# Kernel tuning notes

Hardware: AMD Instinct MI355X
Metric: run time of the kernel (lower is better)

## Reference

```python
import jax, jax.numpy as jnp
import numpy as np
from jax import lax

EPS = 1e-8

def _cosine_cost(x, y):
    # 1 - cosine_similarity over feature dim: [B,N,M]
    xn = x / jnp.clip(jnp.linalg.norm(x, axis=-1, keepdims=True), EPS)
    yn = y / jnp.clip(jnp.linalg.norm(y, axis=-1, keepdims=True), EPS)
    return 1.0 - jnp.einsum('bnd,bmd->bnm', xn, yn)

def _dtw_table(cost):
    # cost: [B,N,M] -> cumulative cost tc: [B,N,M]
    # tc[i,j] = cost[i,j] + min(tc[i-1,j-1], tc[i-1,j], tc[i,j-1])
    B, N, M = cost.shape
    row0 = jnp.cumsum(cost[:, 0, :], axis=1)  # [B,M]

    def col_step(left, inp):
        c, pdiag, pup = inp  # each [B]
        v = c + jnp.minimum(jnp.minimum(pdiag, pup), left)
        return v, v

    def row_step(prev, cost_row):
        # prev, cost_row: [B,M]
        first = prev[:, 0] + cost_row[:, 0]  # [B]
        xs = (cost_row[:, 1:].T, prev[:, :-1].T, prev[:, 1:].T)  # [M-1,B]
        _, rest = lax.scan(col_step, first, xs)  # [M-1,B]
        row = jnp.concatenate([first[:, None], rest.T], axis=1)  # [B,M]
        return row, row

    _, rows = lax.scan(row_step, row0, jnp.swapaxes(cost[:, 1:, :], 0, 1))
    tc = jnp.concatenate([row0[:, None, :], jnp.swapaxes(rows, 0, 1)], axis=1)
    return tc

def _backtrack(tc):
    # tc: [N,M] -> 0/1 path matrix [N,M]; tie-break diag > up > left,
    # matching the torch equality-chain order.
    N, M = tc.shape
    path0 = jnp.zeros((N, M), tc.dtype).at[N - 1, M - 1].set(1.0)

    def cond(s):
        i, j, _ = s
        return jnp.logical_and(i > 0, j > 0)

    def body(s):
        i, j, p = s
        a = tc[i - 1, j - 1]
        b = tc[i - 1, j]
        c = tc[i, j - 1]
        diag = jnp.logical_and(a <= b, a <= c)
        up = jnp.logical_and(jnp.logical_not(diag), b <= c)
        ni = jnp.where(jnp.logical_or(diag, up), i - 1, i)
        nj = jnp.where(jnp.logical_or(diag, jnp.logical_not(up)), j - 1, j)
        p = p.at[ni, nj].set(1.0)
        return ni, nj, p

    _, _, p = lax.while_loop(cond, body, (jnp.int32(N - 1), jnp.int32(M - 1), path0))
    return p.at[0, 0].set(1.0)

def setup_inputs() -> dict:
    key = jax.random.key(0)
    kx, ky = jax.random.split(key)
    B, N, M, D = 64, 512, 512, 256
    x = jax.random.normal(kx, (B, N, D), dtype=jnp.float32)
    y = jax.random.normal(ky, (B, M, D), dtype=jnp.float32)
    return {"x": x, "y": y}

def reference(x, y):
    cost = _cosine_cost(x, y)                 # [B,N,M]
    tc = _dtw_table(cost)                     # [B,N,M]
    path = jax.vmap(_backtrack)(tc)           # [B,N,M]
    pos = jax.nn.logsumexp(jnp.sum(cost * path, axis=1), axis=1)  # [B]
    neg = jax.nn.logsumexp(jnp.sum(cost, axis=1), axis=1)         # [B]
    return pos - neg
```

## Files before the change

### kernel.cpp

```cpp
#include <hip/hip_runtime.h>
#include <hip/hip_bf16.h>
#include <stdint.h>

typedef __attribute__((ext_vector_type(8))) short short8v;
typedef __attribute__((ext_vector_type(4))) float float4v;
typedef __attribute__((ext_vector_type(4))) unsigned short ushort4v;
typedef __attribute__((ext_vector_type(4))) unsigned int uint4v;

#define FINF __builtin_huge_valf()
#define BB 64
#define NN 512
#define DD 256
#define TT_SKEW 768


static __device__ __forceinline__ unsigned short f2bf(float f) {
  union { float f; uint32_t u; } a; a.f = f;
  uint32_t r = a.u + 0x7fffu + ((a.u >> 16) & 1u);
  return (unsigned short)(r >> 16);
}
static __device__ __forceinline__ float bf2f(uint16_t v) {
  return __uint_as_float(((uint32_t)v) << 16);
}

__global__ __launch_bounds__(256) void zero_colsum_kernel(float* __restrict__ colsum)
{
  colsum[blockIdx.x * 256 + threadIdx.x] = 0.0f;
}

__global__ __launch_bounds__(256) void norm_cast_kernel(
    const float* __restrict__ x, const float* __restrict__ y,
    uint16_t* __restrict__ xnb, uint16_t* __restrict__ ynb)
{
  const int wave = threadIdx.x >> 6, lane = threadIdx.x & 63;
  const int row = blockIdx.x * 4 + wave;
  const float* src; uint16_t* dst;
  if (row < BB * NN) { src = x + (size_t)row * DD;            dst = xnb + (size_t)row * DD; }
  else               { src = y + (size_t)(row - BB*NN) * DD;  dst = ynb + (size_t)(row - BB*NN) * DD; }
  const float4v v = *(const float4v*)(src + lane * 4);
  float s = v[0]*v[0] + v[1]*v[1] + v[2]*v[2] + v[3]*v[3];
  #pragma unroll
  for (int d = 1; d < 64; d <<= 1) s += __shfl_xor(s, d, 64);
  const float inv = 1.0f / fmaxf(sqrtf(s), 1e-8f);
  ushort4v o;
  o[0] = f2bf(v[0] * inv); o[1] = f2bf(v[1] * inv);
  o[2] = f2bf(v[2] * inv); o[3] = f2bf(v[3] * inv);
  *(ushort4v*)(dst + lane * 4) = o;
}

__global__ __launch_bounds__(256) void gemm_cost_kernel(
    const uint16_t* __restrict__ xnb, const uint16_t* __restrict__ ynb,
    uint16_t* __restrict__ skew, float* __restrict__ colsum)
{
  __shared__ uint16_t As[128 * 32];
  __shared__ uint16_t Bs[128 * 32];
  const int bid = blockIdx.x;
  const int b = bid >> 4, tm = (bid >> 2) & 3, tn = bid & 3;
  const int tid = threadIdx.x, wave = tid >> 6, lane = tid & 63;
  const int wr = wave >> 1, wc = wave & 1;

  const char* Ab = (const char*)(xnb + (size_t)b * NN * DD + (size_t)tm * 128 * DD);
  const char* Bb = (const char*)(ynb + (size_t)b * NN * DD + (size_t)tn * 128 * DD);

  float4v acc[4][4];
  #pragma unroll
  for (int i = 0; i < 4; i++)
    #pragma unroll
    for (int j = 0; j < 4; j++) acc[i][j] = (float4v){0.f, 0.f, 0.f, 0.f};

  const int seg0 = wave * 2;
  const int o0 = seg0 * 1024 + lane * 16;
  const int o1 = o0 + 1024;
  const int r0 = o0 >> 6, c0 = o0 & 63;
  const int r1 = o1 >> 6, c1 = o1 & 63;

  for (int kk = 0; kk < 8; kk++) {
    const int kb = kk * 64;
    __builtin_amdgcn_global_load_lds(
        (const __attribute__((address_space(1))) uint32_t*)(Ab + (size_t)r0 * 512 + kb + c0),
        (__attribute__((address_space(3))) uint32_t*)((char*)As + seg0 * 1024), 16, 0, 0);
    __builtin_amdgcn_global_load_lds(
        (const __attribute__((address_space(1))) uint32_t*)(Ab + (size_t)r1 * 512 + kb + c1),
        (__attribute__((address_space(3))) uint32_t*)((char*)As + (seg0 + 1) * 1024), 16, 0, 0);
    __builtin_amdgcn_global_load_lds(
        (const __attribute__((address_space(1))) uint32_t*)(Bb + (size_t)r0 * 512 + kb + c0),
        (__attribute__((address_space(3))) uint32_t*)((char*)Bs + seg0 * 1024), 16, 0, 0);
    __builtin_amdgcn_global_load_lds(
        (const __attribute__((address_space(1))) uint32_t*)(Bb + (size_t)r1 * 512 + kb + c1),
        (__attribute__((address_space(3))) uint32_t*)((char*)Bs + (seg0 + 1) * 1024), 16, 0, 0);
    __syncthreads();

    short8v af[4], bfr[4];
    #pragma unroll
    for (int mi = 0; mi < 4; mi++) {
      const int rr = wr * 64 + mi * 16 + (lane & 15);
      af[mi] = *(const short8v*)((const char*)As + rr * 64 + (lane >> 4) * 16);
    }
    #pragma unroll
    for (int nj = 0; nj < 4; nj++) {
      const int rr = wc * 64 + nj * 16 + (lane & 15);
      bfr[nj] = *(const short8v*)((const char*)Bs + rr * 64 + (lane >> 4) * 16);
    }
    #pragma unroll
    for (int mi = 0; mi < 4; mi++)
      #pragma unroll
      for (int nj = 0; nj < 4; nj++)
        acc[mi][nj] = __builtin_amdgcn_mfma_f32_16x16x32_bf16(af[mi], bfr[nj], acc[mi][nj], 0, 0, 0);
    __syncthreads();
  }

  uint16_t* Cb = skew + (size_t)b * TT_SKEW * NN;
  #pragma unroll
  for (int mi = 0; mi < 4; mi++)
    #pragma unroll
    for (int nj = 0; nj < 4; nj++) {
      const int cc = tn * 128 + wc * 64 + nj * 16 + (lane & 15);
      const int lg = cc >> 3;
      #pragma unroll
      for (int v = 0; v < 4; v++) {
        const int rr = tm * 128 + wr * 64 + mi * 16 + (lane >> 4) * 4 + v;
        Cb[(size_t)(rr + 4 * lg) * NN + cc] = f2bf(1.0f - acc[mi][nj][v]);
      }
    }

  #pragma unroll
  for (int nj = 0; nj < 4; nj++) {
    const int cc = tn * 128 + wc * 64 + nj * 16 + (lane & 15);
    float s = 0.f;
    #pragma unroll
    for (int mi = 0; mi < 4; mi++)
      #pragma unroll
      for (int v = 0; v < 4; v++) s += 1.0f - acc[mi][nj][v];
    s += __shfl_xor(s, 16, 64);
    s += __shfl_xor(s, 32, 64);
    if (lane < 16) atomicAdd(&colsum[b * 512 + cc], s);
  }
}

__global__ __launch_bounds__(64, 1) void dtw_fwd_kernel(
    const uint16_t* __restrict__ skew, uint32_t* __restrict__ decg,
    uint32_t* __restrict__ dumpg)
{
  const int l = threadIdx.x;
  const int b = blockIdx.x;
  const uint16_t* csk = skew + (size_t)b * TT_SKEW * NN;
  uint32_t* const dw = decg + (size_t)b * 16384;
  const uint64_t base64 = (uint64_t)(uintptr_t)csk + 16u * (uint32_t)l;
  const bool is0 = (l == 0);

  uint4v rg[4][4];
  #pragma unroll
  for (int i = 0; i < 4; ++i)
    #pragma unroll
    for (int k = 0; k < 4; ++k) {
      const uint64_t a = base64 + ((uint64_t)(4 * i + k) << 10);
      asm volatile("global_load_dwordx4 %0, %1, off" : "=v"(rg[i][k]) : "v"(a));
    }

  float tp[8];
  #pragma unroll
  for (int c = 0; c < 8; ++c) tp[c] = FINF;
  float cl0 = FINF, cl1 = FINF, cl2 = FINF, cl3 = FINF, carry = FINF;

  auto UNPACK = [&](const uint4v R, float (&S)[8]) {
    const float a0 = __uint_as_float(R[0] << 16);
    const float a1 = __uint_as_float(R[0] & 0xFFFF0000u);
    const float a2 = __uint_as_float(R[1] << 16);
    const float a3 = __uint_as_float(R[1] & 0xFFFF0000u);
    const float a4 = __uint_as_float(R[2] << 16);
    const float a5 = __uint_as_float(R[2] & 0xFFFF0000u);
    const float a6 = __uint_as_float(R[3] << 16);
    const float a7 = __uint_as_float(R[3] & 0xFFFF0000u);
    S[0] = a0; S[1] = S[0] + a1; S[2] = S[1] + a2; S[3] = S[2] + a3;
    S[4] = S[3] + a4; S[5] = S[4] + a5; S[6] = S[5] + a6; S[7] = S[6] + a7;
  };

  auto ROW = [&](const float (&S)[8], float (&up)[8], float leftv, float diag0,
                 uint32_t &word, int sh) {
    float dcp[8], mu[8], w[8], PW[8], tn[8];
    dcp[0] = diag0;
    #pragma unroll
    for (int c = 1; c < 8; ++c) dcp[c] = up[c - 1];
    #pragma unroll
    for (int c = 0; c < 8; ++c) mu[c] = fminf(dcp[c], up[c]);
    w[0] = mu[0];
    #pragma unroll
    for (int c = 1; c < 8; ++c) w[c] = mu[c] - S[c - 1];
    PW[0] = w[0];
    #pragma unroll
    for (int c = 1; c < 8; ++c) PW[c] = fminf(PW[c - 1], w[c]);
    #pragma unroll
    for (int c = 0; c < 8; ++c) tn[c] = fminf(PW[c], leftv) + S[c];
    float lc[8];
    lc[0] = leftv;
    #pragma unroll
    for (int c = 1; c < 8; ++c) lc[c] = tn[c - 1];
    #pragma unroll
    for (int c = 0; c < 8; ++c) {
      const uint32_t e = (up[c] < dcp[c]) ? 1u : 0u;
      const uint32_t d = (lc[c] < mu[c]) ? 2u : e;
      word |= d << (sh + 2 * c);
    }
    #pragma unroll
    for (int c = 0; c < 8; ++c) up[c] = tn[c];
  };

  auto STEP = [&](int t, const uint4v R0, const uint4v R1,
                  const uint4v R2, const uint4v R3) {
    const float s0r = __shfl_up(cl0, 1, 64);
    const float s1r = __shfl_up(cl1, 1, 64);
    const float s2r = __shfl_up(cl2, 1, 64);
    const float s3r = __shfl_up(cl3, 1, 64);
    float S0[8], S1[8], S2[8], S3[8];
    UNPACK(R0, S0); UNPACK(R1, S1); UNPACK(R2, S2); UNPACK(R3, S3);
    const float sh0 = is0 ? ((t == 0) ? 0.0f : FINF) : s0r;
    const float sh1 = is0 ? FINF : s1r;
    const float sh2 = is0 ? FINF : s2r;
    const float sh3 = is0 ? FINF : s3r;
    const float dgA = carry;
    const float dg1 = is0 ? FINF : s0r;
    const float dg2 = is0 ? FINF : s1r;
    const float dg3 = is0 ? FINF : s2r;
    carry = sh3;

    const uint32_t a = (uint32_t)(t - l);
    const bool valid = a < 128u;

    float up[8];
    #pragma unroll
    for (int c = 0; c < 8; ++c) up[c] = tp[c];
    uint32_t w0 = 0, w1 = 0;
    ROW(S0, up, sh0, dgA, w0, 0);  const float h0 = up[7];
    ROW(S1, up, sh1, dg1, w0, 16); const float h1 = up[7];
    ROW(S2, up, sh2, dg2, w1, 0);  const float h2 = up[7];
    ROW(S3, up, sh3, dg3, w1, 16); const float h3 = up[7];

    uint32_t* p0 = valid ? (dw + (a << 7) + l) : (dumpg + l);
    uint32_t* p1 = valid ? (dw + (a << 7) + 64 + l) : (dumpg + 64 + l);
    *p0 = w0; *p1 = w1;

    #pragma unroll
    for (int c = 0; c < 8; ++c) tp[c] = valid ? up[c] : tp[c];
    cl0 = valid ? h0 : cl0;
    cl1 = valid ? h1 : cl1;
    cl2 = valid ? h2 : cl2;
    cl3 = valid ? h3 : cl3;
  };

  auto RELOAD = [&](int u, int t) {
    int rr = 4 * (t + 4); if (rr > 764) rr = 764;
    #pragma unroll
    for (int k = 0; k < 4; ++k) {
      const uint64_t a = base64 + ((uint64_t)(rr + k) << 10);
      asm volatile("global_load_dwordx4 %0, %1, off" : "=v"(rg[u][k]) : "v"(a));
    }
  };

  asm volatile("s_waitcnt vmcnt(12)"
               : "+v"(rg[0][0]), "+v"(rg[0][1]), "+v"(rg[0][2]), "+v"(rg[0][3]) : : "memory");
  STEP(0, rg[0][0], rg[0][1], rg[0][2], rg[0][3]); RELOAD(0, 0);
  asm volatile("s_waitcnt vmcnt(14)"
               : "+v"(rg[1][0]), "+v"(rg[1][1]), "+v"(rg[1][2]), "+v"(rg[1][3]) : : "memory");
  STEP(1, rg[1][0], rg[1][1], rg[1][2], rg[1][3]); RELOAD(1, 1);
  asm volatile("s_waitcnt vmcnt(16)"
               : "+v"(rg[2][0]), "+v"(rg[2][1]), "+v"(rg[2][2]), "+v"(rg[2][3]) : : "memory");
  STEP(2, rg[2][0], rg[2][1], rg[2][2], rg[2][3]); RELOAD(2, 2);
  asm volatile("s_waitcnt vmcnt(18)"
               : "+v"(rg[3][0]), "+v"(rg[3][1]), "+v"(rg[3][2]), "+v"(rg[3][3]) : : "memory");
  STEP(3, rg[3][0], rg[3][1], rg[3][2], rg[3][3]); RELOAD(3, 3);

  for (int t0 = 4; t0 < 192; t0 += 4) {
    #pragma unroll
    for (int u = 0; u < 4; ++u) {
      const int t = t0 + u;
      asm volatile("s_waitcnt vmcnt(18)"
                   : "+v"(rg[u][0]), "+v"(rg[u][1]), "+v"(rg[u][2]), "+v"(rg[u][3]) : : "memory");
      STEP(t, rg[u][0], rg[u][1], rg[u][2], rg[u][3]);
      RELOAD(u, t);
    }
  }
  asm volatile("s_waitcnt vmcnt(0)" ::: "memory");
}

__global__ __launch_bounds__(256, 1) void dtw_bt_kernel(
    const uint16_t* __restrict__ skew, const uint32_t* __restrict__ decg,
    const float* __restrict__ colsum, float* __restrict__ out)
{
  extern __shared__ char lds_raw[];
  uint16_t* rlo    = (uint16_t*)(lds_raw + 65536);
  uint16_t* rhi    = (uint16_t*)(lds_raw + 66560);
  float*    colpos = (float*)  (lds_raw + 67584);
  float*    sm     = (float*)  (lds_raw + 69632);
  const uint32_t* dec32 = (const uint32_t*)lds_raw;

  const int tid = threadIdx.x, wave = tid >> 6, lane = tid & 63;
  const int b = blockIdx.x;
  const uint16_t* csk = skew + (size_t)b * TT_SKEW * NN;
  const uint32_t* dg = decg + (size_t)b * 16384;

  #pragma unroll
  for (int i = 0; i < 16; ++i)
    *(uint4v*)(lds_raw + i * 4096 + tid * 16) = *(const uint4v*)(dg + i * 1024 + tid * 4);
  for (int r = tid; r < NN; r += 256) { rlo[r] = 1; rhi[r] = 0; colpos[r] = 0.0f; }

  const float* cs = colsum + (size_t)b * 512;
  const float n0 = cs[tid], n1 = cs[tid + 256];
  float m = fmaxf(n0, n1);
  #pragma unroll
  for (int d = 1; d < 64; d <<= 1) m = fmaxf(m, __shfl_xor(m, d, 64));
  if (lane == 0) sm[wave] = m;
  __syncthreads();
  m = fmaxf(fmaxf(sm[0], sm[1]), fmaxf(sm[2], sm[3]));
  float e = expf(n0 - m) + expf(n1 - m);
  #pragma unroll
  for (int d = 1; d < 64; d <<= 1) e += __shfl_xor(e, d, 64);
  if (lane == 0) sm[4 + wave] = e;
  __syncthreads();
  const float neg = m + logf(sm[4] + sm[5] + sm[6] + sm[7]);
  __syncthreads();

  if (tid == 0) {
    int i = NN - 1, j = NN - 1, hicur = NN - 1;
    while (i > 0 && j > 0) {
      const int a = i >> 2, g2 = j >> 3;
      const uint32_t w0 = dec32[a * 128 + g2];
      const uint32_t w1 = dec32[a * 128 + 64 + g2];
      const int ilo = a << 2, jlo = g2 << 3;
      while (i >= ilo && j >= jlo && i > 0 && j > 0) {
        const uint32_t w = (i & 2) ? w1 : w0;
        const uint32_t dd = (w >> (((i & 1) << 4) + ((j & 7) << 1))) & 3u;
        if (dd == 2u) { j--; }
        else {
          rlo[i] = (uint16_t)j; rhi[i] = (uint16_t)hicur;
          i--;
          if (dd == 0u) j--;
          hicur = j;
        }
      }
    }
    rlo[i] = (uint16_t)j; rhi[i] = (uint16_t)hicur;
  }
  __syncthreads();

  for (int r = tid; r < NN; r += 256) {
    const int lo = rlo[r], hi = rhi[r];
    for (int j = lo; j <= hi; j++) {
      const float cv = bf2f(csk[(size_t)(r + 4 * (j >> 3)) * NN + j]);
      atomicAdd(&colpos[j], cv);
    }
  }
  if (tid == 0 && rlo[0] != 0) atomicAdd(&colpos[0], bf2f(csk[0]));
  __syncthreads();

  const float mv0 = colpos[tid], mv1 = colpos[tid + 256];
  float mx = fmaxf(mv0, mv1);
  #pragma unroll
  for (int d = 1; d < 64; d <<= 1) mx = fmaxf(mx, __shfl_xor(mx, d, 64));
  if (lane == 0) sm[wave] = mx;
  __syncthreads();
  mx = fmaxf(fmaxf(sm[0], sm[1]), fmaxf(sm[2], sm[3]));
  float e2 = expf(mv0 - mx) + expf(mv1 - mx);
  #pragma unroll
  for (int d = 1; d < 64; d <<= 1) e2 += __shfl_xor(e2, d, 64);
  if (lane == 0) sm[4 + wave] = e2;
  __syncthreads();
  if (tid == 0) out[b] = mx + logf(sm[4] + sm[5] + sm[6] + sm[7]) - neg;
}

extern "C" void kernel_launch(void* const* d_in, const int* in_sizes, int n_in,
                              void* d_out, int out_size, void* d_ws, size_t ws_size,
                              hipStream_t stream)
{
  (void)in_sizes; (void)n_in; (void)out_size; (void)ws_size;
  const float* x = (const float*)d_in[0];
  const float* y = (const float*)d_in[1];
  float* out = (float*)d_out;
  char* ws = (char*)d_ws;
  uint16_t* xnb   = (uint16_t*)ws;
  uint16_t* ynb   = (uint16_t*)(ws + (size_t)16777216);
  uint16_t* skew  = (uint16_t*)(ws + (size_t)33554432);
  float*   colsum = (float*)   (ws + (size_t)83886080);
  uint32_t* dumpg = (uint32_t*)(ws + (size_t)84017152);
  uint32_t* decg  = (uint32_t*)(ws + (size_t)84021248);

  (void)hipFuncSetAttribute((const void*)dtw_bt_kernel,
                            hipFuncAttributeMaxDynamicSharedMemorySize, 69760);

  zero_colsum_kernel<<<128, 256, 0, stream>>>(colsum);
  norm_cast_kernel<<<16384, 256, 0, stream>>>(x, y, xnb, ynb);
  gemm_cost_kernel<<<1024, 256, 0, stream>>>(xnb, ynb, skew, colsum);
  dtw_fwd_kernel<<<64, 64, 0, stream>>>(skew, decg, dumpg);
  dtw_bt_kernel<<<64, 256, 69760, stream>>>(skew, decg, colsum, out);
}
```

Before: 285.6 us.

## Fuse DTW forward and backtrack kernels, keeping direction bits in LDS

Merges the DTW forward-pass kernel and the backtrack/logsumexp kernel into one 64-thread kernel per batch. The direction bits now go straight to shared memory instead of a global buffer, which removes a kernel launch and the global write and re-read of the 64KB decision table per batch. The reductions are reworked for a single wave using shuffles only. The tradeoffs are that the final path-cost gather runs with 64 threads instead of 256, and the load-wait schedule is simplified to a uniform vmcnt(12) with the memory clobber dropped.

```diff
diff --git a/kernel.cpp b/kernel.cpp
--- a/kernel.cpp
+++ b/kernel.cpp
@@ -137,14 +137,14 @@
   }
 }
 
-__global__ __launch_bounds__(64, 1) void dtw_fwd_kernel(
-    const uint16_t* __restrict__ skew, uint32_t* __restrict__ decg,
-    uint32_t* __restrict__ dumpg)
-{
+__global__ __launch_bounds__(64, 1) void dtw_fwdbt_kernel(
+    const uint16_t* __restrict__ skew, const float* __restrict__ colsum,
+    float* __restrict__ out)
+{
+  extern __shared__ char lds_raw[];
   const int l = threadIdx.x;
   const int b = blockIdx.x;
   const uint16_t* csk = skew + (size_t)b * TT_SKEW * NN;
-  uint32_t* const dw = decg + (size_t)b * 16384;
   const uint64_t base64 = (uint64_t)(uintptr_t)csk + 16u * (uint32_t)l;
   const bool is0 = (l == 0);
 
@@ -235,9 +235,10 @@
     ROW(S2, up, sh2, dg2, w1, 0);  const float h2 = up[7];
     ROW(S3, up, sh3, dg3, w1, 16); const float h3 = up[7];
 
-    uint32_t* p0 = valid ? (dw + (a << 7) + l) : (dumpg + l);
-    uint32_t* p1 = valid ? (dw + (a << 7) + 64 + l) : (dumpg + 64 + l);
-    *p0 = w0; *p1 = w1;
+    const uint32_t byte0 = valid ? ((a << 9) | (((uint32_t)l) << 2))
+                                 : (65536u | (((uint32_t)l) << 2));
+    *(uint32_t*)(lds_raw + byte0) = w0;
+    *(uint32_t*)(lds_raw + byte0 + 256) = w1;
 
     #pragma unroll
     for (int c = 0; c < 8; ++c) tp[c] = valid ? up[c] : tp[c];
@@ -256,70 +257,41 @@
     }
   };
 
-  asm volatile("s_waitcnt vmcnt(12)"
-               : "+v"(rg[0][0]), "+v"(rg[0][1]), "+v"(rg[0][2]), "+v"(rg[0][3]) : : "memory");
-  STEP(0, rg[0][0], rg[0][1], rg[0][2], rg[0][3]); RELOAD(0, 0);
-  asm volatile("s_waitcnt vmcnt(14)"
-               : "+v"(rg[1][0]), "+v"(rg[1][1]), "+v"(rg[1][2]), "+v"(rg[1][3]) : : "memory");
-  STEP(1, rg[1][0], rg[1][1], rg[1][2], rg[1][3]); RELOAD(1, 1);
-  asm volatile("s_waitcnt vmcnt(16)"
-               : "+v"(rg[2][0]), "+v"(rg[2][1]), "+v"(rg[2][2]), "+v"(rg[2][3]) : : "memory");
-  STEP(2, rg[2][0], rg[2][1], rg[2][2], rg[2][3]); RELOAD(2, 2);
-  asm volatile("s_waitcnt vmcnt(18)"
-               : "+v"(rg[3][0]), "+v"(rg[3][1]), "+v"(rg[3][2]), "+v"(rg[3][3]) : : "memory");
-  STEP(3, rg[3][0], rg[3][1], rg[3][2], rg[3][3]); RELOAD(3, 3);
-
-  for (int t0 = 4; t0 < 192; t0 += 4) {
+  for (int t0 = 0; t0 < 192; t0 += 4) {
     #pragma unroll
     for (int u = 0; u < 4; ++u) {
       const int t = t0 + u;
-      asm volatile("s_waitcnt vmcnt(18)"
-                   : "+v"(rg[u][0]), "+v"(rg[u][1]), "+v"(rg[u][2]), "+v"(rg[u][3]) : : "memory");
+      asm volatile("s_waitcnt vmcnt(12)"
+                   : "+v"(rg[u][0]), "+v"(rg[u][1]), "+v"(rg[u][2]), "+v"(rg[u][3]));
       STEP(t, rg[u][0], rg[u][1], rg[u][2], rg[u][3]);
       RELOAD(u, t);
     }
   }
   asm volatile("s_waitcnt vmcnt(0)" ::: "memory");
-}
-
-__global__ __launch_bounds__(256, 1) void dtw_bt_kernel(
-    const uint16_t* __restrict__ skew, const uint32_t* __restrict__ decg,
-    const float* __restrict__ colsum, float* __restrict__ out)
-{
-  extern __shared__ char lds_raw[];
-  uint16_t* rlo    = (uint16_t*)(lds_raw + 65536);
-  uint16_t* rhi    = (uint16_t*)(lds_raw + 66560);
-  float*    colpos = (float*)  (lds_raw + 67584);
-  float*    sm     = (float*)  (lds_raw + 69632);
+
+  uint16_t* rlo    = (uint16_t*)(lds_raw + 66048);
+  uint16_t* rhi    = (uint16_t*)(lds_raw + 67072);
+  float*    colpos = (float*)  (lds_raw + 68096);
   const uint32_t* dec32 = (const uint32_t*)lds_raw;
 
-  const int tid = threadIdx.x, wave = tid >> 6, lane = tid & 63;
-  const int b = blockIdx.x;
-  const uint16_t* csk = skew + (size_t)b * TT_SKEW * NN;
-  const uint32_t* dg = decg + (size_t)b * 16384;
-
-  #pragma unroll
-  for (int i = 0; i < 16; ++i)
-    *(uint4v*)(lds_raw + i * 4096 + tid * 16) = *(const uint4v*)(dg + i * 1024 + tid * 4);
-  for (int r = tid; r < NN; r += 256) { rlo[r] = 1; rhi[r] = 0; colpos[r] = 0.0f; }
+  for (int r = l; r < NN; r += 64) { rlo[r] = 1; rhi[r] = 0; colpos[r] = 0.0f; }
 
   const float* cs = colsum + (size_t)b * 512;
-  const float n0 = cs[tid], n1 = cs[tid + 256];
-  float m = fmaxf(n0, n1);
+  float nv[8];
+  float m = -FINF;
+  #pragma unroll
+  for (int k = 0; k < 8; ++k) { nv[k] = cs[l + 64 * k]; m = fmaxf(m, nv[k]); }
   #pragma unroll
   for (int d = 1; d < 64; d <<= 1) m = fmaxf(m, __shfl_xor(m, d, 64));
-  if (lane == 0) sm[wave] = m;
+  float e = 0.f;
+  #pragma unroll
+  for (int k = 0; k < 8; ++k) e += expf(nv[k] - m);
+  #pragma unroll
+  for (int d = 1; d < 64; d <<= 1) e += __shfl_xor(e, d, 64);
+  const float neg = m + logf(e);
   __syncthreads();
-  m = fmaxf(fmaxf(sm[0], sm[1]), fmaxf(sm[2], sm[3]));
-  float e = expf(n0 - m) + expf(n1 - m);
-  #pragma unroll
-  for (int d = 1; d < 64; d <<= 1) e += __shfl_xor(e, d, 64);
-  if (lane == 0) sm[4 + wave] = e;
-  __syncthreads();
-  const float neg = m + logf(sm[4] + sm[5] + sm[6] + sm[7]);
-  __syncthreads();
-
-  if (tid == 0) {
+
+  if (l == 0) {
     int i = NN - 1, j = NN - 1, hicur = NN - 1;
     while (i > 0 && j > 0) {
       const int a = i >> 2, g2 = j >> 3;
@@ -342,29 +314,30 @@
   }
   __syncthreads();
 
-  for (int r = tid; r < NN; r += 256) {
+  for (int r = l; r < NN; r += 64) {
     const int lo = rlo[r], hi = rhi[r];
     for (int j = lo; j <= hi; j++) {
       const float cv = bf2f(csk[(size_t)(r + 4 * (j >> 3)) * NN + j]);
       atomicAdd(&colpos[j], cv);
     }
   }
-  if (tid == 0 && rlo[0] != 0) atomicAdd(&colpos[0], bf2f(csk[0]));
+  if (l == 0 && rlo[0] != 0) atomicAdd(&colpos[0], bf2f(csk[0]));
   __syncthreads();
 
-  const float mv0 = colpos[tid], mv1 = colpos[tid + 256];
-  float mx = fmaxf(mv0, mv1);
-  #pragma unroll
-  for (int d = 1; d < 64; d <<= 1) mx = fmaxf(mx, __shfl_xor(mx, d, 64));
-  if (lane == 0) sm[wave] = mx;
-  __syncthreads();
-  mx = fmaxf(fmaxf(sm[0], sm[1]), fmaxf(sm[2], sm[3]));
-  float e2 = expf(mv0 - mx) + expf(mv1 - mx);
-  #pragma unroll
-  for (int d = 1; d < 64; d <<= 1) e2 += __shfl_xor(e2, d, 64);
-  if (lane == 0) sm[4 + wave] = e2;
-  __syncthreads();
-  if (tid == 0) out[b] = mx + logf(sm[4] + sm[5] + sm[6] + sm[7]) - neg;
+  float mv[8];
+  float mx2 = -FINF;
+  #pragma unroll
+  for (int k = 0; k < 8; k++) { mv[k] = colpos[l + 64 * k]; mx2 = fmaxf(mx2, mv[k]); }
+  #pragma unroll
+  for (int d = 1; d < 64; d <<= 1) mx2 = fmaxf(mx2, __shfl_xor(mx2, d, 64));
+  float se2 = 0.f;
+  #pragma unroll
+  for (int k = 0; k < 8; k++) se2 += expf(mv[k] - mx2);
+  #pragma unroll
+  for (int d = 1; d < 64; d <<= 1) se2 += __shfl_xor(se2, d, 64);
+  const float pos = mx2 + logf(se2);
+
+  if (l == 0) out[b] = pos - neg;
 }
 
 extern "C" void kernel_launch(void* const* d_in, const int* in_sizes, int n_in,
@@ -380,15 +353,12 @@
   uint16_t* ynb   = (uint16_t*)(ws + (size_t)16777216);
   uint16_t* skew  = (uint16_t*)(ws + (size_t)33554432);
   float*   colsum = (float*)   (ws + (size_t)83886080);
-  uint32_t* dumpg = (uint32_t*)(ws + (size_t)84017152);
-  uint32_t* decg  = (uint32_t*)(ws + (size_t)84021248);
-
-  (void)hipFuncSetAttribute((const void*)dtw_bt_kernel,
-                            hipFuncAttributeMaxDynamicSharedMemorySize, 69760);
+
+  (void)hipFuncSetAttribute((const void*)dtw_fwdbt_kernel,
+                            hipFuncAttributeMaxDynamicSharedMemorySize, 70144);
 
   zero_colsum_kernel<<<128, 256, 0, stream>>>(colsum);
   norm_cast_kernel<<<16384, 256, 0, stream>>>(x, y, xnb, ynb);
   gemm_cost_kernel<<<1024, 256, 0, stream>>>(xnb, ynb, skew, colsum);
-  dtw_fwd_kernel<<<64, 64, 0, stream>>>(skew, decg, dumpg);
-  dtw_bt_kernel<<<64, 256, 69760, stream>>>(skew, decg, colsum, out);
-}
+  dtw_fwdbt_kernel<<<64, 64, 70144, stream>>>(skew, colsum, out);
+}
```

Result: no change. 280.4 us (-1.8%).
